# Optimization experiments

Hardware: AMD Instinct MI355X
Metric: run time of the kernel (lower is better)

## Reference

```python
import jax, jax.numpy as jnp
import numpy as np

LN_EPS = 1e-12
CHEB_K = 3
HIDDEN = 64


def _layernorm(x, w, b):
    m = jnp.mean(x, axis=-1, keepdims=True)
    v = jnp.mean((x - m) ** 2, axis=-1, keepdims=True)
    return (x - m) / jnp.sqrt(v + LN_EPS) * w + b


def _magcn(x, node_emb, time_emb, ln_w, ln_b, W_pool, b_pool):
    # x: [B,N,C]; node_emb: [N,D]; W_pool: [D,K,C,O]; b_pool: [D,O]
    e = _layernorm(node_emb + time_emb[None, :], ln_w, ln_b)  # dropout = identity (eval)
    supports = jax.nn.softmax(e @ e.T, axis=1)                # [N,N]
    N = e.shape[0]
    Ts = [jnp.eye(N, dtype=x.dtype), supports]
    for _ in range(2, CHEB_K):
        Ts.append(2.0 * supports @ Ts[-1] - Ts[-2])
    S = jnp.stack(Ts, axis=0)                                 # [K,N,N]
    weights = jnp.einsum('nd,dkio->nkio', e, W_pool)          # [N,K,C,O]
    bias = e @ b_pool                                         # [N,O]
    x_g = jnp.einsum('knm,bmc->bnkc', S, x)                   # [B,N,K,C]
    return jnp.einsum('bnki,nkio->bno', x_g, weights) + bias  # [B,N,O]


def setup_inputs() -> dict:
    key = jax.random.key(0)
    ks = jax.random.split(key, 10)
    B, N, C, H, D = 64, 1024, 64, HIDDEN, 16
    return {
        'x': jax.random.normal(ks[0], (B, N, C), jnp.float32),
        'norm_dis_matrix': jax.random.uniform(ks[1], (N, N), jnp.float32),
        'state': jax.random.normal(ks[2], (B, N, H), jnp.float32),
        'node_embeddings': jax.random.normal(ks[3], (N, D), jnp.float32),
        'node_flows': jax.random.normal(ks[4], (B, N), jnp.float32),
        'time_embeddings': jax.random.normal(ks[5], (D,), jnp.float32),
        'gate_W': jax.random.normal(ks[6], (D, CHEB_K, C + H, 2 * H), jnp.float32) * 0.1,
        'gate_b': jax.random.normal(ks[7], (D, 2 * H), jnp.float32) * 0.1,
        'gate_ln_w': jnp.ones((D,), jnp.float32),
        'gate_ln_b': jnp.zeros((D,), jnp.float32),
        'update_W': jax.random.normal(ks[8], (D, CHEB_K, C + H, H), jnp.float32) * 0.1,
        'update_b': jax.random.normal(ks[9], (D, H), jnp.float32) * 0.1,
        'update_ln_w': jnp.ones((D,), jnp.float32),
        'update_ln_b': jnp.zeros((D,), jnp.float32),
    }


def reference(x, norm_dis_matrix, state, node_embeddings, node_flows, time_embeddings,
              gate_W, gate_b, gate_ln_w, gate_ln_b,
              update_W, update_b, update_ln_w, update_ln_b):
    inp_state = jnp.concatenate([x, state], axis=-1)  # [B,N,C+H]
    z_r = jax.nn.sigmoid(_magcn(inp_state, node_embeddings, time_embeddings,
                                gate_ln_w, gate_ln_b, gate_W, gate_b))
    z, r = z_r[..., :HIDDEN], z_r[..., HIDDEN:]
    candidate = jnp.concatenate([x, z * state], axis=-1)
    hc = jnp.tanh(_magcn(candidate, node_embeddings, time_embeddings,
                         update_ln_w, update_ln_b, update_W, update_b))
    return r * state + (1.0 - r) * hc
```

## Files before the change

kernel.cpp:

```cpp
#include <hip/hip_runtime.h>
#include <hip/hip_bf16.h>

typedef __hip_bfloat16 bf16;
typedef __attribute__((ext_vector_type(8))) short bf16x8;
typedef __attribute__((ext_vector_type(4))) float f32x4;

constexpr int Bn = 64;
constexpr int Nn = 1024;
constexpr int Dd = 16;
constexpr int Cc = 64;
constexpr int Hh = 64;
constexpr int CI = 128;
constexpr int OG = 128;
constexpr int OU = 64;
constexpr int Jt = Bn * CI;

__device__ __forceinline__ float b2f(bf16 v) { return __bfloat162float(v); }
__device__ __forceinline__ float lo2f(unsigned u) { return __uint_as_float(u << 16); }
__device__ __forceinline__ float hi2f(unsigned u) { return __uint_as_float(u & 0xffff0000u); }
__device__ __forceinline__ float bfbits2f(unsigned short u) { return __uint_as_float(((unsigned)u) << 16); }
__device__ __forceinline__ unsigned short f2bfbits(float x) {
    bf16 h = __float2bfloat16(x);
    return *reinterpret_cast<unsigned short*>(&h);
}

__device__ __forceinline__ float ldin(const void* p, size_t i, int flag) {
    return flag ? b2f(((const bf16*)p)[i]) : ((const float*)p)[i];
}

__device__ __forceinline__ void gload_lds16(const void* g, void* l) {
    __builtin_amdgcn_global_load_lds((const __attribute__((address_space(1))) void*)g,
                                     (__attribute__((address_space(3))) void*)l, 16, 0, 0);
}

__global__ void detect_kernel(const void* glnw, int* flag) {
    unsigned u = *(const unsigned*)glnw;
    *flag = (u == 0x3F800000u) ? 0 : 1;
}

__global__ void conv_f32(const void* __restrict__ src, float* __restrict__ dst,
                         int n, const int* __restrict__ flag) {
    const int f = *flag;
    for (int i = blockIdx.x * blockDim.x + threadIdx.x; i < n; i += gridDim.x * blockDim.x)
        dst[i] = ldin(src, i, f);
}
__global__ void conv_bf(const void* __restrict__ src, bf16* __restrict__ dst,
                        int n, const int* __restrict__ flag) {
    const int f = *flag;
    for (int i = blockIdx.x * blockDim.x + threadIdx.x; i < n; i += gridDim.x * blockDim.x)
        dst[i] = f ? ((const bf16*)src)[i] : __float2bfloat16(((const float*)src)[i]);
}

__global__ void ln_kernel(const void* __restrict__ nemb, const void* __restrict__ temb,
                          const void* __restrict__ wg, const void* __restrict__ bg,
                          const void* __restrict__ wu, const void* __restrict__ bu,
                          float* __restrict__ e_g, float* __restrict__ e_u,
                          const int* __restrict__ flag) {
    const int f = *flag;
    int t = blockIdx.x * blockDim.x + threadIdx.x;
    if (t >= 2 * Nn) return;
    int which = t >> 10;
    int n = t & (Nn - 1);
    float v[Dd];
    float mean = 0.f;
#pragma unroll
    for (int d = 0; d < Dd; d++) { v[d] = ldin(nemb, n * Dd + d, f) + ldin(temb, d, f); mean += v[d]; }
    mean *= (1.f / Dd);
    float var = 0.f;
#pragma unroll
    for (int d = 0; d < Dd; d++) { float c = v[d] - mean; var += c * c; }
    var *= (1.f / Dd);
    float inv = 1.f / sqrtf(var + 1e-12f);
    const void* w = which ? wu : wg;
    const void* bb = which ? bu : bg;
    float* e = which ? e_u : e_g;
#pragma unroll
    for (int d = 0; d < Dd; d++)
        e[n * Dd + d] = (v[d] - mean) * inv * ldin(w, d, f) + ldin(bb, d, f);
}

__global__ __launch_bounds__(256) void attn_kernel(const float* __restrict__ e, bf16* __restrict__ A) {
    __shared__ float en[Dd];
    __shared__ float logits[Nn];
    __shared__ float red[256];
    const int n = blockIdx.x, t = threadIdx.x;
    if (t < Dd) en[t] = e[n * Dd + t];
    __syncthreads();
    float lmax = -1e30f;
    for (int m = t; m < Nn; m += 256) {
        float s = 0.f;
#pragma unroll
        for (int d = 0; d < Dd; d++) s += en[d] * e[m * Dd + d];
        logits[m] = s;
        lmax = fmaxf(lmax, s);
    }
    red[t] = lmax; __syncthreads();
    for (int s = 128; s > 0; s >>= 1) { if (t < s) red[t] = fmaxf(red[t], red[t + s]); __syncthreads(); }
    const float M = red[0];
    __syncthreads();
    float lsum = 0.f;
    for (int m = t; m < Nn; m += 256) { float p = expf(logits[m] - M); logits[m] = p; lsum += p; }
    red[t] = lsum; __syncthreads();
    for (int s = 128; s > 0; s >>= 1) { if (t < s) red[t] += red[t + s]; __syncthreads(); }
    const float inv = 1.f / red[0];
    for (int m = t; m < Nn; m += 256) A[(size_t)n * Nn + m] = __float2bfloat16(logits[m] * inv);
}

__global__ __launch_bounds__(256) void build_xg0(const void* __restrict__ x, const void* __restrict__ oth,
                                                 bf16* __restrict__ xg0t, bf16* __restrict__ xg0s,
                                                 const int* __restrict__ flag, int oth_bf16) {
    const int f = *flag;
    const int b = blockIdx.x;
    const int n0 = blockIdx.y * 64;
    __shared__ bf16 tile[128][68];
    const int t = threadIdx.x;
#pragma unroll
    for (int idx = t; idx < 64 * 128; idx += 256) {
        const int n = idx >> 7, i = idx & 127;
        const size_t base = ((size_t)b << 10) + n0 + n;
        float v;
        if (i < Cc) v = ldin(x, base * Cc + i, f);
        else v = oth_bf16 ? b2f(((const bf16*)oth)[base * Hh + i - Cc])
                          : ldin(oth, base * Hh + i - Cc, f);
        tile[i][n] = __float2bfloat16(v);
        xg0s[base * CI + i] = tile[i][n];
    }
    __syncthreads();
#pragma unroll
    for (int idx = t; idx < 128 * 64; idx += 256) {
        const int i = idx >> 6, n = idx & 63;
        xg0t[((size_t)(b * CI + i) << 10) + n0 + n] = tile[i][n];
    }
}

__global__ __launch_bounds__(256) void agg_mfma(const bf16* __restrict__ Amat,
                                                const bf16* __restrict__ Xmat,
                                                const bf16* __restrict__ Sub,
                                                bf16* __restrict__ Ct,
                                                bf16* __restrict__ Cs,
                                                int cheb, int write_t) {
    __shared__ bf16 Atile[128 * 32];
    __shared__ bf16 Xtile[128 * 32];
    char* AtileC = (char*)Atile;
    char* XtileC = (char*)Xtile;

    const int t = threadIdx.x;
    const int lane = t & 63, w = t >> 6;
    const int j0 = blockIdx.x * 128;
    const int m0 = blockIdx.y * 128;
    const int wr = (w >> 1) * 64, wc = (w & 1) * 64;
    const int lr = lane & 15, lq = lane >> 4;

    f32x4 acc[4][4];
#pragma unroll
    for (int a = 0; a < 4; a++)
#pragma unroll
        for (int b = 0; b < 4; b++) acc[a][b] = (f32x4){0.f, 0.f, 0.f, 0.f};

    const int srow = w * 16 + (lane >> 2);
    const int scb = (lane & 3) * 16;

    for (int k0 = 0; k0 < Nn; k0 += 32) {
        __syncthreads();
#pragma unroll
        for (int p = 0; p < 2; p++) {
            const int row = p * 64 + srow;
            gload_lds16((const char*)Amat + (size_t)(m0 + row) * 2048 + k0 * 2 + scb,
                        AtileC + p * 4096 + w * 1024);
            gload_lds16((const char*)Xmat + (size_t)(j0 + row) * 2048 + k0 * 2 + scb,
                        XtileC + p * 4096 + w * 1024);
        }
        __syncthreads();
        bf16x8 af[4], xf[4];
#pragma unroll
        for (int fr = 0; fr < 4; fr++)
            af[fr] = *(const bf16x8*)(AtileC + (wr + fr * 16 + lr) * 64 + lq * 16);
#pragma unroll
        for (int fc = 0; fc < 4; fc++)
            xf[fc] = *(const bf16x8*)(XtileC + (wc + fc * 16 + lr) * 64 + lq * 16);
#pragma unroll
        for (int fr = 0; fr < 4; fr++)
#pragma unroll
            for (int fc = 0; fc < 4; fc++)
                acc[fr][fc] = __builtin_amdgcn_mfma_f32_16x16x32_bf16(af[fr], xf[fc], acc[fr][fc], 0, 0, 0);
    }

#pragma unroll
    for (int fr = 0; fr < 4; fr++) {
        const int m = m0 + wr + fr * 16 + lq * 4;
#pragma unroll
        for (int fc = 0; fc < 4; fc++) {
            const int j = j0 + wc + fc * 16 + lr;
            f32x4 v = acc[fr][fc];
            const size_t off = ((size_t)j << 10) + m;
            if (cheb) {
                const ushort4 s = *(const ushort4*)((const unsigned short*)Sub + off);
                v.x = 2.f * v.x - bfbits2f(s.x);
                v.y = 2.f * v.y - bfbits2f(s.y);
                v.z = 2.f * v.z - bfbits2f(s.z);
                v.w = 2.f * v.w - bfbits2f(s.w);
            }
            ushort4 o4;
            o4.x = f2bfbits(v.x); o4.y = f2bfbits(v.y); o4.z = f2bfbits(v.z); o4.w = f2bfbits(v.w);
            if (write_t) *(ushort4*)((unsigned short*)Ct + off) = o4;
            const int b = j >> 7, i = j & 127;
            unsigned short* ps = (unsigned short*)Cs;
            const unsigned short* pv = (const unsigned short*)&o4;
#pragma unroll
            for (int q = 0; q < 4; q++)
                ps[((((size_t)b << 10) + m + q) << 7) + i] = pv[q];
        }
    }
}

constexpr int WROWB = 272;

__global__ __launch_bounds__(256, 2) void pernode_gemm(
    const bf16* __restrict__ x0, const bf16* __restrict__ x1, const bf16* __restrict__ x2,
    const float* __restrict__ e, const unsigned short* __restrict__ Wb,
    const float* __restrict__ bpool,
    const void* __restrict__ state, const float* __restrict__ r_in,
    bf16* __restrict__ zs, float* __restrict__ r_out, void* __restrict__ out,
    const int* __restrict__ flag, int OSTR, int two_per_node, int is_upd)
{
    const int f = *flag;
    const int bx = blockIdx.x;
    const int n = two_per_node ? (bx >> 1) : bx;
    const int obase = two_per_node ? ((bx & 1) << 6) : 0;

    __shared__ bf16 Xc[64 * 128];
    __shared__ bf16 Whi[64 * (WROWB / 2)];
    __shared__ bf16 Wlo[64 * (WROWB / 2)];
    __shared__ float enS[16];
    __shared__ float biasS[64];
    char* XcC = (char*)Xc;
    char* WhiC = (char*)Whi;
    char* WloC = (char*)Wlo;

    const int t = threadIdx.x;
    const int lane = t & 63, w = t >> 6;
    const int lr = lane & 15, lq = lane >> 4;

    if (t < 16) enS[t] = e[n * 16 + t];
    __syncthreads();
    if (t < 64) {
        float s = 0.f;
#pragma unroll
        for (int d = 0; d < 16; d++) s += enS[d] * bpool[d * OSTR + obase + t];
        biasS[t] = s;
    }
    float enr[16];
#pragma unroll
    for (int d = 0; d < 16; d++) enr[d] = enS[d];

    const int krow0 = (t >> 4) * 8;
    const int ocol = (t & 15) * 4;

    f32x4 acc[4];
#pragma unroll
    for (int i = 0; i < 4; i++) acc[i] = (f32x4){0.f, 0.f, 0.f, 0.f};

    const bf16* xs[3] = {x0, x1, x2};

    for (int ch = 0; ch < 3; ch++) {
        __syncthreads();
        {
            const bf16* Xsrc = xs[ch];
#pragma unroll
            for (int p = 0; p < 4; p++) {
                const int row = p * 16 + w * 4 + (lane >> 4);
                const int colg = (lane & 15) ^ (row & 7);
                gload_lds16(Xsrc + (((size_t)row << 10) + n) * 128 + colg * 8,
                            XcC + (p * 16 + w * 4) * 256);
            }
        }
        float wacc[8][4];
#pragma unroll
        for (int r = 0; r < 8; r++)
#pragma unroll
            for (int c = 0; c < 4; c++) wacc[r][c] = 0.f;
        {
            const unsigned short* wp0 = Wb + (size_t)(ch * 128 + krow0) * OSTR + obase + ocol;
#pragma unroll 2
            for (int d = 0; d < 16; d++) {
                const unsigned short* wp = wp0 + (size_t)d * 384 * OSTR;
                const float ed = enr[d];
#pragma unroll
                for (int r = 0; r < 8; r++) {
                    const uint2 u = *(const uint2*)(wp + r * OSTR);
                    wacc[r][0] += ed * lo2f(u.x);
                    wacc[r][1] += ed * hi2f(u.x);
                    wacc[r][2] += ed * lo2f(u.y);
                    wacc[r][3] += ed * hi2f(u.y);
                }
            }
        }
        __syncthreads();
#pragma unroll
        for (int c = 0; c < 4; c++) {
            unsigned short hbuf[8], lbuf[8];
#pragma unroll
            for (int r = 0; r < 8; r++) {
                const float v = wacc[r][c];
                const unsigned short h = f2bfbits(v);
                hbuf[r] = h;
                lbuf[r] = f2bfbits(v - bfbits2f(h));
            }
            uint4 hv, lv;
            hv.x = hbuf[0] | ((unsigned)hbuf[1] << 16);
            hv.y = hbuf[2] | ((unsigned)hbuf[3] << 16);
            hv.z = hbuf[4] | ((unsigned)hbuf[5] << 16);
            hv.w = hbuf[6] | ((unsigned)hbuf[7] << 16);
            lv.x = lbuf[0] | ((unsigned)lbuf[1] << 16);
            lv.y = lbuf[2] | ((unsigned)lbuf[3] << 16);
            lv.z = lbuf[4] | ((unsigned)lbuf[5] << 16);
            lv.w = lbuf[6] | ((unsigned)lbuf[7] << 16);
            *(uint4*)(WhiC + (ocol + c) * WROWB + krow0 * 2) = hv;
            *(uint4*)(WloC + (ocol + c) * WROWB + krow0 * 2) = lv;
        }
        __syncthreads();
#pragma unroll
        for (int ks = 0; ks < 4; ks++) {
            bf16x8 af;
            {
                const int row = w * 16 + lr;
                const int col16 = (ks * 4 + lq) ^ (row & 7);
                af = *(const bf16x8*)(XcC + row * 256 + col16 * 16);
            }
#pragma unroll
            for (int fc = 0; fc < 4; fc++) {
                const bf16x8 bh = *(const bf16x8*)(WhiC + (fc * 16 + lr) * WROWB + ks * 64 + lq * 16);
                acc[fc] = __builtin_amdgcn_mfma_f32_16x16x32_bf16(af, bh, acc[fc], 0, 0, 0);
            }
#pragma unroll
            for (int fc = 0; fc < 4; fc++) {
                const bf16x8 bl = *(const bf16x8*)(WloC + (fc * 16 + lr) * WROWB + ks * 64 + lq * 16);
                acc[fc] = __builtin_amdgcn_mfma_f32_16x16x32_bf16(af, bl, acc[fc], 0, 0, 0);
            }
        }
    }

#pragma unroll
    for (int fc = 0; fc < 4; fc++) {
        const int ol = fc * 16 + lr;
        const float bias = biasS[ol];
#pragma unroll
        for (int q = 0; q < 4; q++) {
            const int b = w * 16 + lq * 4 + q;
            const size_t idx = (((size_t)b << 10) + n) * 64 + ol;
            const float v = acc[fc][q] + bias;
            if (is_upd) {
                const float hc = tanhf(v);
                const float r = r_in[idx];
                const float st = ldin(state, idx, f);
                const float o = r * st + (1.f - r) * hc;
                if (f) ((bf16*)out)[idx] = __float2bfloat16(o);
                else   ((float*)out)[idx] = o;
            } else {
                const float sg = 1.f / (1.f + expf(-v));
                if (obase == 0) {
                    const float st = ldin(state, idx, f);
                    zs[idx] = __float2bfloat16(sg * st);
                } else {
                    r_out[idx] = sg;
                }
            }
        }
    }
}

extern "C" void kernel_launch(void* const* d_in, const int* in_sizes, int n_in,
                              void* d_out, int out_size, void* d_ws, size_t ws_size,
                              hipStream_t stream) {
    const void* x     = d_in[0];
    const void* state = d_in[2];
    const void* nemb  = d_in[3];
    const void* temb  = d_in[5];
    const void* gW    = d_in[6];
    const void* gb    = d_in[7];
    const void* glnw  = d_in[8];
    const void* glnb  = d_in[9];
    const void* uW    = d_in[10];
    const void* ub    = d_in[11];
    const void* ulnw  = d_in[12];
    const void* ulnb  = d_in[13];

    constexpr int GW_N = Dd * 3 * CI * OG;
    constexpr int GB_N = Dd * OG;
    constexpr int UW_N = Dd * 3 * CI * OU;
    constexpr int UB_N = Dd * OU;

    char* base = (char*)d_ws;
    size_t off = 0;
    auto carve = [&](size_t bytes) { char* p = base + off; off += (bytes + 255) & ~(size_t)255; return p; };
    int*   flag = (int*)carve(4);
    unsigned short* gWb = (unsigned short*)carve(GW_N * 2);
    unsigned short* uWb = (unsigned short*)carve(UW_N * 2);
    float* gbf = (float*)carve(GB_N * 4);
    float* ubf = (float*)carve(UB_N * 4);
    float* e_g = (float*)carve(Nn * Dd * 4);
    float* e_u = (float*)carve(Nn * Dd * 4);
    bf16*  Abf  = (bf16*)carve((size_t)Nn * Nn * 2);
    bf16*  xg0t = (bf16*)carve((size_t)Jt * Nn * 2);
    bf16*  xg0s = (bf16*)carve((size_t)Jt * Nn * 2);
    bf16*  xg1t = (bf16*)carve((size_t)Jt * Nn * 2);
    bf16*  xg1s = (bf16*)carve((size_t)Jt * Nn * 2);
    bf16*  xg2s = (bf16*)carve((size_t)Jt * Nn * 2);
    bf16*  zs   = (bf16*)carve((size_t)Bn * Nn * Hh * 2);
    float* r_s  = (float*)carve((size_t)Bn * Nn * Hh * 4);
    if (ws_size < off) return;

    detect_kernel<<<1, 1, 0, stream>>>(glnw, flag);
    conv_bf<<<(GW_N + 255) / 256, 256, 0, stream>>>(gW, (bf16*)gWb, GW_N, flag);
    conv_bf<<<(UW_N + 255) / 256, 256, 0, stream>>>(uW, (bf16*)uWb, UW_N, flag);
    conv_f32<<<(GB_N + 255) / 256, 256, 0, stream>>>(gb, gbf, GB_N, flag);
    conv_f32<<<(UB_N + 255) / 256, 256, 0, stream>>>(ub, ubf, UB_N, flag);
    ln_kernel<<<8, 256, 0, stream>>>(nemb, temb, glnw, glnb, ulnw, ulnb, e_g, e_u, flag);

    attn_kernel<<<Nn, 256, 0, stream>>>(e_g, Abf);
    build_xg0<<<dim3(Bn, 16), 256, 0, stream>>>(x, state, xg0t, xg0s, flag, 0);
    agg_mfma<<<dim3(Jt / 128, Nn / 128), 256, 0, stream>>>(Abf, xg0t, nullptr, xg1t, xg1s, 0, 1);
    agg_mfma<<<dim3(Jt / 128, Nn / 128), 256, 0, stream>>>(Abf, xg1t, xg0t, xg1t, xg2s, 1, 0);
    pernode_gemm<<<2 * Nn, 256, 0, stream>>>(xg0s, xg1s, xg2s, e_g, gWb, gbf,
                                             state, nullptr, zs, r_s, nullptr, flag, OG, 1, 0);

    attn_kernel<<<Nn, 256, 0, stream>>>(e_u, Abf);
    build_xg0<<<dim3(Bn, 16), 256, 0, stream>>>(x, zs, xg0t, xg0s, flag, 1);
    agg_mfma<<<dim3(Jt / 128, Nn / 128), 256, 0, stream>>>(Abf, xg0t, nullptr, xg1t, xg1s, 0, 1);
    agg_mfma<<<dim3(Jt / 128, Nn / 128), 256, 0, stream>>>(Abf, xg1t, xg0t, xg1t, xg2s, 1, 0);
    pernode_gemm<<<Nn, 256, 0, stream>>>(xg0s, xg1s, xg2s, e_u, uWb, ubf,
                                         state, r_s, nullptr, nullptr, d_out, flag, OU, 0, 1);
}
```

Baseline: 486.1 us.

## Process two nodes per block in pernode_gemm with transposed weights in registers

The pooled weights are pre-transposed to a [D,O,K] layout so each thread can load 8 contiguous k values and build its MFMA B-fragments directly in registers. This removes the LDS staging of the hi/lo weight split and two barriers per chunk. Each block now handles two nodes, so every weight load is reused for both nodes' embeddings and the grid halves. Occupancy hint rises to 3. The X tile in LDS doubles and register pressure grows, which may limit occupancy.

After: 570.3 us. +17.3%, slower.

```diff
diff --git a/kernel.cpp b/kernel.cpp
--- a/kernel.cpp
+++ b/kernel.cpp
@@ -44,11 +44,23 @@
     for (int i = blockIdx.x * blockDim.x + threadIdx.x; i < n; i += gridDim.x * blockDim.x)
         dst[i] = ldin(src, i, f);
 }
-__global__ void conv_bf(const void* __restrict__ src, bf16* __restrict__ dst,
-                        int n, const int* __restrict__ flag) {
+
+__global__ __launch_bounds__(256) void wtrans(const void* __restrict__ src, unsigned short* __restrict__ Wt,
+                                              int O, int osh, const int* __restrict__ flag) {
     const int f = *flag;
-    for (int i = blockIdx.x * blockDim.x + threadIdx.x; i < n; i += gridDim.x * blockDim.x)
-        dst[i] = f ? ((const bf16*)src)[i] : __float2bfloat16(((const float*)src)[i]);
+    const int k0 = blockIdx.x * 64;
+    const int d = blockIdx.y;
+    __shared__ unsigned short tile[64][136];
+    const int t = threadIdx.x;
+    for (int idx = t; idx < 64 * O; idx += 256) {
+        const int kk = idx >> osh, o = idx & (O - 1);
+        tile[kk][o] = f2bfbits(ldin(src, ((size_t)d * 384 + k0 + kk) * O + o, f));
+    }
+    __syncthreads();
+    for (int idx = t; idx < O * 64; idx += 256) {
+        const int o = idx >> 6, kk = idx & 63;
+        Wt[((size_t)d * O + o) * 384 + k0 + kk] = tile[kk][o];
+    }
 }
 
 __global__ void ln_kernel(const void* __restrict__ nemb, const void* __restrict__ temb,
@@ -213,156 +225,129 @@
     }
 }
 
-constexpr int WROWB = 272;
-
-__global__ __launch_bounds__(256, 2) void pernode_gemm(
+__global__ __launch_bounds__(256, 3) void pernode_gemm(
     const bf16* __restrict__ x0, const bf16* __restrict__ x1, const bf16* __restrict__ x2,
-    const float* __restrict__ e, const unsigned short* __restrict__ Wb,
+    const float* __restrict__ e, const unsigned short* __restrict__ Wt,
     const float* __restrict__ bpool,
     const void* __restrict__ state, const float* __restrict__ r_in,
     bf16* __restrict__ zs, float* __restrict__ r_out, void* __restrict__ out,
-    const int* __restrict__ flag, int OSTR, int two_per_node, int is_upd)
+    const int* __restrict__ flag, int OSTR, int gate)
 {
     const int f = *flag;
     const int bx = blockIdx.x;
-    const int n = two_per_node ? (bx >> 1) : bx;
-    const int obase = two_per_node ? ((bx & 1) << 6) : 0;
-
-    __shared__ bf16 Xc[64 * 128];
-    __shared__ bf16 Whi[64 * (WROWB / 2)];
-    __shared__ bf16 Wlo[64 * (WROWB / 2)];
-    __shared__ float enS[16];
-    __shared__ float biasS[64];
+    const int np = gate ? (bx >> 1) : bx;
+    const int obase = gate ? ((bx & 1) << 6) : 0;
+    const int n0 = np * 2, n1 = n0 + 1;
+
+    __shared__ bf16 Xc[2 * 64 * 128];
     char* XcC = (char*)Xc;
-    char* WhiC = (char*)Whi;
-    char* WloC = (char*)Wlo;
 
     const int t = threadIdx.x;
     const int lane = t & 63, w = t >> 6;
     const int lr = lane & 15, lq = lane >> 4;
-
-    if (t < 16) enS[t] = e[n * 16 + t];
-    __syncthreads();
-    if (t < 64) {
-        float s = 0.f;
-#pragma unroll
-        for (int d = 0; d < 16; d++) s += enS[d] * bpool[d * OSTR + obase + t];
-        biasS[t] = s;
-    }
-    float enr[16];
-#pragma unroll
-    for (int d = 0; d < 16; d++) enr[d] = enS[d];
-
-    const int krow0 = (t >> 4) * 8;
-    const int ocol = (t & 15) * 4;
-
-    f32x4 acc[4];
-#pragma unroll
-    for (int i = 0; i < 4; i++) acc[i] = (f32x4){0.f, 0.f, 0.f, 0.f};
+    const int og = obase + w * 16 + lr;
+
+    float en0[16], en1[16];
+#pragma unroll
+    for (int d = 0; d < 16; d++) { en0[d] = e[n0 * 16 + d]; en1[d] = e[n1 * 16 + d]; }
+
+    f32x4 acc0[4], acc1[4];
+#pragma unroll
+    for (int i = 0; i < 4; i++) { acc0[i] = (f32x4){0.f,0.f,0.f,0.f}; acc1[i] = (f32x4){0.f,0.f,0.f,0.f}; }
 
     const bf16* xs[3] = {x0, x1, x2};
+    const size_t dstr = (size_t)OSTR * 384;
+    const unsigned short* wbase = Wt + (size_t)og * 384;
 
     for (int ch = 0; ch < 3; ch++) {
         __syncthreads();
         {
             const bf16* Xsrc = xs[ch];
 #pragma unroll
-            for (int p = 0; p < 4; p++) {
-                const int row = p * 16 + w * 4 + (lane >> 4);
-                const int colg = (lane & 15) ^ (row & 7);
-                gload_lds16(Xsrc + (((size_t)row << 10) + n) * 128 + colg * 8,
-                            XcC + (p * 16 + w * 4) * 256);
+            for (int p = 0; p < 8; p++) {
+                const int r = w * 32 + p * 4 + (lane >> 4);
+                const int nd = r >> 6;
+                const int b = r & 63;
+                const int g = (lane & 15) ^ (r & 15);
+                gload_lds16(Xsrc + (((size_t)b << 10) + (nd ? n1 : n0)) * 128 + g * 8,
+                            XcC + (w * 32 + p * 4) * 256);
             }
         }
-        float wacc[8][4];
-#pragma unroll
-        for (int r = 0; r < 8; r++)
-#pragma unroll
-            for (int c = 0; c < 4; c++) wacc[r][c] = 0.f;
-        {
-            const unsigned short* wp0 = Wb + (size_t)(ch * 128 + krow0) * OSTR + obase + ocol;
-#pragma unroll 2
+        for (int ks = 0; ks < 4; ks++) {
+            float w0[8], w1[8];
+#pragma unroll
+            for (int j = 0; j < 8; j++) { w0[j] = 0.f; w1[j] = 0.f; }
+            const unsigned short* wp = wbase + ch * 128 + ks * 32 + lq * 8;
+#pragma unroll 8
             for (int d = 0; d < 16; d++) {
-                const unsigned short* wp = wp0 + (size_t)d * 384 * OSTR;
-                const float ed = enr[d];
-#pragma unroll
-                for (int r = 0; r < 8; r++) {
-                    const uint2 u = *(const uint2*)(wp + r * OSTR);
-                    wacc[r][0] += ed * lo2f(u.x);
-                    wacc[r][1] += ed * hi2f(u.x);
-                    wacc[r][2] += ed * lo2f(u.y);
-                    wacc[r][3] += ed * hi2f(u.y);
-                }
+                const uint4 u = *(const uint4*)(wp + (size_t)d * dstr);
+                const float v0 = lo2f(u.x), v1 = hi2f(u.x), v2 = lo2f(u.y), v3 = hi2f(u.y);
+                const float v4 = lo2f(u.z), v5 = hi2f(u.z), v6 = lo2f(u.w), v7 = hi2f(u.w);
+                const float a = en0[d], b = en1[d];
+                w0[0] += a * v0; w0[1] += a * v1; w0[2] += a * v2; w0[3] += a * v3;
+                w0[4] += a * v4; w0[5] += a * v5; w0[6] += a * v6; w0[7] += a * v7;
+                w1[0] += b * v0; w1[1] += b * v1; w1[2] += b * v2; w1[3] += b * v3;
+                w1[4] += b * v4; w1[5] += b * v5; w1[6] += b * v6; w1[7] += b * v7;
+            }
+            union U8 { bf16x8 v; unsigned short s[8]; } bh0, bl0, bh1, bl1;
+#pragma unroll
+            for (int j = 0; j < 8; j++) {
+                unsigned short h = f2bfbits(w0[j]);
+                bh0.s[j] = h; bl0.s[j] = f2bfbits(w0[j] - bfbits2f(h));
+                h = f2bfbits(w1[j]);
+                bh1.s[j] = h; bl1.s[j] = f2bfbits(w1[j] - bfbits2f(h));
+            }
+            if (ks == 0) __syncthreads();
+#pragma unroll
+            for (int mf = 0; mf < 4; mf++) {
+                const int row = mf * 16 + lr;
+                const int blk = (ks * 4 + lq) ^ lr;
+                const bf16x8 af0 = *(const bf16x8*)(XcC + row * 256 + blk * 16);
+                const bf16x8 af1 = *(const bf16x8*)(XcC + (64 + row) * 256 + blk * 16);
+                acc0[mf] = __builtin_amdgcn_mfma_f32_16x16x32_bf16(af0, bh0.v, acc0[mf], 0, 0, 0);
+                acc0[mf] = __builtin_amdgcn_mfma_f32_16x16x32_bf16(af0, bl0.v, acc0[mf], 0, 0, 0);
+                acc1[mf] = __builtin_amdgcn_mfma_f32_16x16x32_bf16(af1, bh1.v, acc1[mf], 0, 0, 0);
+                acc1[mf] = __builtin_amdgcn_mfma_f32_16x16x32_bf16(af1, bl1.v, acc1[mf], 0, 0, 0);
             }
         }
-        __syncthreads();
-#pragma unroll
-        for (int c = 0; c < 4; c++) {
-            unsigned short hbuf[8], lbuf[8];
-#pragma unroll
-            for (int r = 0; r < 8; r++) {
-                const float v = wacc[r][c];
-                const unsigned short h = f2bfbits(v);
-                hbuf[r] = h;
-                lbuf[r] = f2bfbits(v - bfbits2f(h));
-            }
-            uint4 hv, lv;
-            hv.x = hbuf[0] | ((unsigned)hbuf[1] << 16);
-            hv.y = hbuf[2] | ((unsigned)hbuf[3] << 16);
-            hv.z = hbuf[4] | ((unsigned)hbuf[5] << 16);
-            hv.w = hbuf[6] | ((unsigned)hbuf[7] << 16);
-            lv.x = lbuf[0] | ((unsigned)lbuf[1] << 16);
-            lv.y = lbuf[2] | ((unsigned)lbuf[3] << 16);
-            lv.z = lbuf[4] | ((unsigned)lbuf[5] << 16);
-            lv.w = lbuf[6] | ((unsigned)lbuf[7] << 16);
-            *(uint4*)(WhiC + (ocol + c) * WROWB + krow0 * 2) = hv;
-            *(uint4*)(WloC + (ocol + c) * WROWB + krow0 * 2) = lv;
-        }
-        __syncthreads();
-#pragma unroll
-        for (int ks = 0; ks < 4; ks++) {
-            bf16x8 af;
-            {
-                const int row = w * 16 + lr;
-                const int col16 = (ks * 4 + lq) ^ (row & 7);
-                af = *(const bf16x8*)(XcC + row * 256 + col16 * 16);
-            }
-#pragma unroll
-            for (int fc = 0; fc < 4; fc++) {
-                const bf16x8 bh = *(const bf16x8*)(WhiC + (fc * 16 + lr) * WROWB + ks * 64 + lq * 16);
-                acc[fc] = __builtin_amdgcn_mfma_f32_16x16x32_bf16(af, bh, acc[fc], 0, 0, 0);
-            }
-#pragma unroll
-            for (int fc = 0; fc < 4; fc++) {
-                const bf16x8 bl = *(const bf16x8*)(WloC + (fc * 16 + lr) * WROWB + ks * 64 + lq * 16);
-                acc[fc] = __builtin_amdgcn_mfma_f32_16x16x32_bf16(af, bl, acc[fc], 0, 0, 0);
-            }
-        }
-    }
-
-#pragma unroll
-    for (int fc = 0; fc < 4; fc++) {
-        const int ol = fc * 16 + lr;
-        const float bias = biasS[ol];
-#pragma unroll
-        for (int q = 0; q < 4; q++) {
-            const int b = w * 16 + lq * 4 + q;
-            const size_t idx = (((size_t)b << 10) + n) * 64 + ol;
-            const float v = acc[fc][q] + bias;
-            if (is_upd) {
-                const float hc = tanhf(v);
-                const float r = r_in[idx];
-                const float st = ldin(state, idx, f);
-                const float o = r * st + (1.f - r) * hc;
-                if (f) ((bf16*)out)[idx] = __float2bfloat16(o);
-                else   ((float*)out)[idx] = o;
-            } else {
-                const float sg = 1.f / (1.f + expf(-v));
-                if (obase == 0) {
+    }
+
+    float bias0 = 0.f, bias1 = 0.f;
+#pragma unroll
+    for (int d = 0; d < 16; d++) {
+        const float bp = bpool[d * OSTR + og];
+        bias0 += en0[d] * bp;
+        bias1 += en1[d] * bp;
+    }
+    const int ol = og & 63;
+
+#pragma unroll
+    for (int nd = 0; nd < 2; nd++) {
+        const int n_ = nd ? n1 : n0;
+        const float bias = nd ? bias1 : bias0;
+#pragma unroll
+        for (int mf = 0; mf < 4; mf++) {
+            const f32x4 a = nd ? acc1[mf] : acc0[mf];
+#pragma unroll
+            for (int q = 0; q < 4; q++) {
+                const int b = mf * 16 + lq * 4 + q;
+                const size_t idx = (((size_t)b << 10) + n_) * 64 + ol;
+                const float v = a[q] + bias;
+                if (gate) {
+                    const float sg = 1.f / (1.f + expf(-v));
+                    if (obase == 0) {
+                        const float st = ldin(state, idx, f);
+                        zs[idx] = __float2bfloat16(sg * st);
+                    } else {
+                        r_out[idx] = sg;
+                    }
+                } else {
+                    const float hc = tanhf(v);
+                    const float r = r_in[idx];
                     const float st = ldin(state, idx, f);
-                    zs[idx] = __float2bfloat16(sg * st);
-                } else {
-                    r_out[idx] = sg;
+                    const float o = r * st + (1.f - r) * hc;
+                    if (f) ((bf16*)out)[idx] = __float2bfloat16(o);
+                    else   ((float*)out)[idx] = o;
                 }
             }
         }
@@ -394,8 +379,8 @@
     size_t off = 0;
     auto carve = [&](size_t bytes) { char* p = base + off; off += (bytes + 255) & ~(size_t)255; return p; };
     int*   flag = (int*)carve(4);
-    unsigned short* gWb = (unsigned short*)carve(GW_N * 2);
-    unsigned short* uWb = (unsigned short*)carve(UW_N * 2);
+    unsigned short* gWt = (unsigned short*)carve(GW_N * 2);
+    unsigned short* uWt = (unsigned short*)carve(UW_N * 2);
     float* gbf = (float*)carve(GB_N * 4);
     float* ubf = (float*)carve(UB_N * 4);
     float* e_g = (float*)carve(Nn * Dd * 4);
@@ -411,8 +396,8 @@
     if (ws_size < off) return;
 
     detect_kernel<<<1, 1, 0, stream>>>(glnw, flag);
-    conv_bf<<<(GW_N + 255) / 256, 256, 0, stream>>>(gW, (bf16*)gWb, GW_N, flag);
-    conv_bf<<<(UW_N + 255) / 256, 256, 0, stream>>>(uW, (bf16*)uWb, UW_N, flag);
+    wtrans<<<dim3(6, 16), 256, 0, stream>>>(gW, gWt, OG, 7, flag);
+    wtrans<<<dim3(6, 16), 256, 0, stream>>>(uW, uWt, OU, 6, flag);
     conv_f32<<<(GB_N + 255) / 256, 256, 0, stream>>>(gb, gbf, GB_N, flag);
     conv_f32<<<(UB_N + 255) / 256, 256, 0, stream>>>(ub, ubf, UB_N, flag);
     ln_kernel<<<8, 256, 0, stream>>>(nemb, temb, glnw, glnb, ulnw, ulnb, e_g, e_u, flag);
@@ -421,13 +406,13 @@
     build_xg0<<<dim3(Bn, 16), 256, 0, stream>>>(x, state, xg0t, xg0s, flag, 0);
     agg_mfma<<<dim3(Jt / 128, Nn / 128), 256, 0, stream>>>(Abf, xg0t, nullptr, xg1t, xg1s, 0, 1);
     agg_mfma<<<dim3(Jt / 128, Nn / 128), 256, 0, stream>>>(Abf, xg1t, xg0t, xg1t, xg2s, 1, 0);
-    pernode_gemm<<<2 * Nn, 256, 0, stream>>>(xg0s, xg1s, xg2s, e_g, gWb, gbf,
-                                             state, nullptr, zs, r_s, nullptr, flag, OG, 1, 0);
+    pernode_gemm<<<Nn, 256, 0, stream>>>(xg0s, xg1s, xg2s, e_g, gWt, gbf,
+                                         state, nullptr, zs, r_s, nullptr, flag, OG, 1);
 
     attn_kernel<<<Nn, 256, 0, stream>>>(e_u, Abf);
     build_xg0<<<dim3(Bn, 16), 256, 0, stream>>>(x, zs, xg0t, xg0s, flag, 1);
     agg_mfma<<<dim3(Jt / 128, Nn / 128), 256, 0, stream>>>(Abf, xg0t, nullptr, xg1t, xg1s, 0, 1);
     agg_mfma<<<dim3(Jt / 128, Nn / 128), 256, 0, stream>>>(Abf, xg1t, xg0t, xg1t, xg2s, 1, 0);
-    pernode_gemm<<<Nn, 256, 0, stream>>>(xg0s, xg1s, xg2s, e_u, uWb, ubf,
-                                         state, r_s, nullptr, nullptr, d_out, flag, OU, 0, 1);
-}
+    pernode_gemm<<<Nn / 2, 256, 0, stream>>>(xg0s, xg1s, xg2s, e_u, uWt, ubf,
+                                             state, r_s, nullptr, nullptr, d_out, flag, OU, 0);
+}
```
